# Performance work log

Measured on AMD Instinct MI355X. Metric: run time of the kernel, lower is better.

Reference implementation:

```python
import jax, jax.numpy as jnp
import numpy as np
from jax import lax

L, B, N, D = 6, 4, 2048, 512
H, DH = 8, 64
ID = H * DH           # 512
M = 266               # int(64*log(64)) random features
INNER = 2 * D         # conformer expansion
K = 31                # depthwise kernel
PAD = (15, 15)        # calc_same_padding(31)
EPS_LN = 1e-5


def setup_inputs() -> dict:
    key = jax.random.key(0)
    ks = jax.random.split(key, 12)
    s = 0.02
    return {
        "x": jax.random.normal(ks[0], (B, N, D), jnp.float32),
        "ln1_g": jnp.ones((L, D), jnp.float32),
        "ln1_b": jnp.zeros((L, D), jnp.float32),
        "wq": jax.random.normal(ks[1], (L, ID, D), jnp.float32) * s,
        "bq": jnp.zeros((L, ID), jnp.float32),
        "wk": jax.random.normal(ks[2], (L, ID, D), jnp.float32) * s,
        "bk": jnp.zeros((L, ID), jnp.float32),
        "wv": jax.random.normal(ks[3], (L, ID, D), jnp.float32) * s,
        "bv": jnp.zeros((L, ID), jnp.float32),
        "wo": jax.random.normal(ks[4], (L, ID, D), jnp.float32) * s,
        "bo": jnp.zeros((L, D), jnp.float32),
        # FAVOR+ random projection buffer (gaussian orthogonal ~ iid gaussian rows)
        "proj": jax.random.normal(ks[5], (L, M, DH), jnp.float32),
        "ln2_g": jnp.ones((L, D), jnp.float32),
        "ln2_b": jnp.zeros((L, D), jnp.float32),
        "pw1_w": jax.random.normal(ks[6], (L, 2 * INNER, D), jnp.float32) * s,
        "pw1_b": jnp.zeros((L, 2 * INNER), jnp.float32),
        "dw_w": jax.random.normal(ks[7], (L, INNER, K), jnp.float32) * s,
        "dw_b": jnp.zeros((L, INNER), jnp.float32),
        "pw2_w": jax.random.normal(ks[8], (L, D, INNER), jnp.float32) * s,
        "pw2_b": jnp.zeros((L, D), jnp.float32),
    }


def layer_norm(x, g, b):
    mu = jnp.mean(x, axis=-1, keepdims=True)
    var = jnp.mean((x - mu) ** 2, axis=-1, keepdims=True)
    return (x - mu) * lax.rsqrt(var + EPS_LN) * g + b


def softmax_kernel(data, proj, is_query, eps=1e-4):
    # data: [b,h,n,dh], proj: [m,dh]
    dn = DH ** -0.25
    ratio = M ** -0.5
    data_dash = jnp.einsum('bhnd,md->bhnm', dn * data, proj)
    diag = jnp.sum(data * data, axis=-1, keepdims=True) * 0.5 * dn * dn  # [b,h,n,1]
    if is_query:
        mx = jnp.max(data_dash, axis=-1, keepdims=True)
        return ratio * (jnp.exp(data_dash - diag - mx) + eps)
    else:
        return ratio * jnp.exp(data_dash - diag + eps)


def favor_attention(q, k, v, proj):
    qp = softmax_kernel(q, proj, True)   # [b,h,n,m]
    kp = softmax_kernel(k, proj, False)  # [b,h,n,m]
    k_cumsum = jnp.sum(kp, axis=-2)      # [b,h,m]
    d_inv = 1.0 / (jnp.einsum('bhnm,bhm->bhn', qp, k_cumsum) + 1e-8)
    context = jnp.einsum('bhnm,bhne->bhme', kp, v)          # [b,h,m,dh]
    out = jnp.einsum('bhme,bhnm,bhn->bhne', context, qp, d_inv)
    return out


def pcmer_forward(x, ln1_g, ln1_b, wq, bq, wk, bk, wv, bv, wo, bo, proj,
                  ln2_g, ln2_b, pw1_w, pw1_b, dw_w, dw_b, pw2_w, pw2_b):
    for l in range(L):
        # --- self attention (FAVOR+) ---
        h = layer_norm(x, ln1_g[l], ln1_b[l])
        q = (h @ wq[l].T + bq[l]).reshape(B, N, H, DH).transpose(0, 2, 1, 3)
        k = (h @ wk[l].T + bk[l]).reshape(B, N, H, DH).transpose(0, 2, 1, 3)
        v = (h @ wv[l].T + bv[l]).reshape(B, N, H, DH).transpose(0, 2, 1, 3)
        o = favor_attention(q, k, v, proj[l])                 # [b,h,n,dh]
        o = o.transpose(0, 2, 1, 3).reshape(B, N, ID)
        x = x + (o @ wo[l].T + bo[l])
        # --- conformer conv module ---
        h = layer_norm(x, ln2_g[l], ln2_b[l])
        y = h @ pw1_w[l].T + pw1_b[l]                         # [b,n,2*inner]
        a, g = y[..., :INNER], y[..., INNER:]
        y = a * jax.nn.sigmoid(g)                             # GLU
        yt = jnp.pad(y.transpose(0, 2, 1), ((0, 0), (0, 0), PAD))  # [b,inner,n+30]
        dw = lax.conv_general_dilated(
            yt, dw_w[l][:, None, :], window_strides=(1,), padding='VALID',
            feature_group_count=INNER,
            dimension_numbers=('NCH', 'OIH', 'NCH')) + dw_b[l][None, :, None]
        dw = jax.nn.silu(dw).transpose(0, 2, 1)               # [b,n,inner]
        x = x + (dw @ pw2_w[l].T + pw2_b[l])
    return x


def reference(x, ln1_g, ln1_b, wq, bq, wk, bk, wv, bv, wo, bo, proj,
              ln2_g, ln2_b, pw1_w, pw1_b, dw_w, dw_b, pw2_w, pw2_b):
    return pcmer_forward(x, ln1_g, ln1_b, wq, bq, wk, bk, wv, bv, wo, bo, proj,
                         ln2_g, ln2_b, pw1_w, pw1_b, dw_w, dw_b, pw2_w, pw2_b)
```

## Files before the change

kernel.cpp:

```cpp
#include <hip/hip_runtime.h>


#define L_LAYERS 6
#define B_ 4
#define N_ 2048
#define D_ 512
#define H_ 8
#define DH_ 64
#define M_ 266
#define INNER_ 1024
#define T_ 8192
#define PS_ 320
#define QKVS_ 1536
#define NS_ 8

typedef __attribute__((ext_vector_type(8))) short short8;
typedef __attribute__((ext_vector_type(4))) float floatx4;

__device__ __forceinline__ ushort f2bf(float f) {
  union { float f; uint u; } v; v.f = f;
  uint r = v.u + 0x7fffu + ((v.u >> 16) & 1u);
  return (ushort)(r >> 16);
}
__device__ __forceinline__ float bf2f(ushort u) {
  union { uint u; float f; } v; v.u = ((uint)u) << 16;
  return v.f;
}
__device__ __forceinline__ float wave_sum(float v) {
#pragma unroll
  for (int m = 1; m < 64; m <<= 1) v += __shfl_xor(v, m);
  return v;
}
__device__ __forceinline__ void async_cp16(const void* g, void* l) {
  __builtin_amdgcn_global_load_lds(
      (const __attribute__((address_space(1))) void*)g,
      (__attribute__((address_space(3))) void*)l, 16, 0, 0);
}

__global__ void f2bf4_kernel(const float4* __restrict__ in, ushort* __restrict__ out, int n4) {
  int i = blockIdx.x * 256 + threadIdx.x;
  if (i < n4) {
    float4 v = in[i];
    ushort4 r;
    r.x = f2bf(v.x); r.y = f2bf(v.y); r.z = f2bf(v.z); r.w = f2bf(v.w);
    *(ushort4*)(out + (size_t)i * 4) = r;
  }
}
__global__ void pack_qkv_w(const float4* __restrict__ src, ushort* __restrict__ dst, int off) {
  int i = blockIdx.x * 256 + threadIdx.x;
  if (i >= L_LAYERS * 512 * 128) return;
  int l = i >> 16;
  int rem = i & 65535;
  int row = rem >> 7, c4 = rem & 127;
  float4 v = src[i];
  ushort4 r;
  r.x = f2bf(v.x); r.y = f2bf(v.y); r.z = f2bf(v.z); r.w = f2bf(v.w);
  *(ushort4*)(dst + ((size_t)l * QKVS_ + off + row) * 512 + c4 * 4) = r;
}
__global__ void pack_qkv_b(const float* __restrict__ bq, const float* __restrict__ bk,
                           const float* __restrict__ bv, float* __restrict__ dst) {
  int i = blockIdx.x * 256 + threadIdx.x;
  if (i >= L_LAYERS * QKVS_) return;
  int l = i / QKVS_, c = i % QKVS_;
  dst[i] = c < 512 ? bq[l * 512 + c] : (c < 1024 ? bk[l * 512 + c - 512] : bv[l * 512 + c - 1024]);
}
__global__ void pad_proj(const float* __restrict__ proj, ushort* __restrict__ dst) {
  int i = blockIdx.x * 256 + threadIdx.x;
  if (i >= L_LAYERS * 320 * 64) return;
  int l = i / (320 * 64), rem = i % (320 * 64), m = rem >> 6, kk = rem & 63;
  dst[i] = (m < M_) ? f2bf(proj[((size_t)l * M_ + m) * 64 + kk]) : (ushort)0;
}
__global__ void pack_pw1_w(const float4* __restrict__ src, ushort* __restrict__ dst) {
  int i = blockIdx.x * 256 + threadIdx.x;
  if (i >= L_LAYERS * 2048 * 128) return;
  int l = i >> 18;
  int rem = i & 262143;
  int cp = rem >> 7, c4 = rem & 127;
  int s = (cp >> 4) & 1;
  int srow = ((cp >> 5) << 4) + (cp & 15) + s * 1024;
  float4 v = src[((size_t)l * 2048 + srow) * 128 + c4];
  ushort4 r;
  r.x = f2bf(v.x); r.y = f2bf(v.y); r.z = f2bf(v.z); r.w = f2bf(v.w);
  *(ushort4*)(dst + ((size_t)l * 2048 + cp) * 512 + c4 * 4) = r;
}
__global__ void pack_pw1_b(const float* __restrict__ src, float* __restrict__ dst) {
  int i = blockIdx.x * 256 + threadIdx.x;
  if (i >= L_LAYERS * 2048) return;
  int l = i >> 11, cp = i & 2047;
  int s = (cp >> 4) & 1;
  int srow = ((cp >> 5) << 4) + (cp & 15) + s * 1024;
  dst[i] = src[l * 2048 + srow];
}

__global__ __launch_bounds__(256) void ln_kernel(const float* __restrict__ x,
                                                 const float* __restrict__ g,
                                                 const float* __restrict__ b,
                                                 ushort* __restrict__ out) {
  const int t = blockIdx.x;
  const int tid = threadIdx.x;
  const float* row = x + (size_t)t * D_;
  float v0 = row[tid], v1 = row[tid + 256];
  float s1 = v0 + v1;
  float s2 = v0 * v0 + v1 * v1;
  s1 = wave_sum(s1);
  s2 = wave_sum(s2);
  __shared__ float sh1[4], sh2[4];
  int w = tid >> 6;
  if ((tid & 63) == 0) { sh1[w] = s1; sh2[w] = s2; }
  __syncthreads();
  s1 = sh1[0] + sh1[1] + sh1[2] + sh1[3];
  s2 = sh2[0] + sh2[1] + sh2[2] + sh2[3];
  float mu = s1 * (1.f / D_);
  float var = s2 * (1.f / D_) - mu * mu;
  float rs = rsqrtf(var + 1e-5f);
  out[(size_t)t * D_ + tid]       = f2bf((v0 - mu) * rs * g[tid] + b[tid]);
  out[(size_t)t * D_ + tid + 256] = f2bf((v1 - mu) * rs * g[tid + 256] + b[tid + 256]);
}

template <bool HAS_RES, bool OUT_BF16, int ACT, int KT>
__global__ __launch_bounds__(256) void gemm_mfma(const ushort* __restrict__ A,
                                                 const ushort* __restrict__ W,
                                                 const float* __restrict__ bias,
                                                 const float* __restrict__ res,
                                                 void* __restrict__ Cout,
                                                 int ldc) {
  constexpr int NT = KT / 32;
  __shared__ ushort As[3][128 * 32];
  __shared__ ushort Bs[3][128 * 32];
  const int tid = threadIdx.x;
  const int w = tid >> 6, lane = tid & 63;
  const int row0 = blockIdx.x * 128, col0 = blockIdx.y * 128;
  const int rl = lane >> 2;
  const int lc = ((lane & 3) ^ ((lane >> 3) & 3)) * 8;
  const ushort* gA0 = A + (size_t)(row0 + w * 32 + rl) * KT + lc;
  const ushort* gA1 = gA0 + (size_t)16 * KT;
  const ushort* gB0 = W + (size_t)(col0 + w * 32 + rl) * KT + lc;
  const ushort* gB1 = gB0 + (size_t)16 * KT;
  const int m16 = lane & 15, quad = lane >> 4;
  const int awr = (w >> 1) * 64, bwc = (w & 1) * 64;
  floatx4 acc[4][4] = {};

  auto stage = [&](int t, int buf) {
    async_cp16(gA0 + t * 32, As[buf] + w * 1024);
    async_cp16(gA1 + t * 32, As[buf] + w * 1024 + 512);
    async_cp16(gB0 + t * 32, Bs[buf] + w * 1024);
    async_cp16(gB1 + t * 32, Bs[buf] + w * 1024 + 512);
  };
  auto body = [&](int buf, bool bar2) {
    short8 af[4], bfr[4];
#pragma unroll
    for (int i = 0; i < 4; i++) {
      int r = awr + i * 16 + m16;
      af[i] = *(const short8*)&As[buf][r * 32 + (quad ^ ((r >> 1) & 3)) * 8];
    }
#pragma unroll
    for (int j = 0; j < 4; j++) {
      int r = bwc + j * 16 + m16;
      bfr[j] = *(const short8*)&Bs[buf][r * 32 + (quad ^ ((r >> 1) & 3)) * 8];
    }
    if (bar2) {
      asm volatile("s_waitcnt lgkmcnt(0)" ::: "memory");
      __builtin_amdgcn_sched_barrier(0);
      __builtin_amdgcn_s_barrier();
    }
#pragma unroll
    for (int i = 0; i < 4; i++)
#pragma unroll
      for (int j = 0; j < 4; j++)
        acc[i][j] = __builtin_amdgcn_mfma_f32_16x16x32_bf16(af[i], bfr[j], acc[i][j], 0, 0, 0);
  };

  stage(0, 0);
  stage(1, 1);
  int c = 0;
  for (int t = 0; t < NT - 2; t++) {
    int pf = c + 2; if (pf >= 3) pf -= 3;
    stage(t + 2, pf);
    asm volatile("s_waitcnt vmcnt(8)" ::: "memory");
    __builtin_amdgcn_s_barrier();
    body(c, true);
    c++; if (c >= 3) c -= 3;
  }
  asm volatile("s_waitcnt vmcnt(4)" ::: "memory");
  __builtin_amdgcn_s_barrier();
  body(c, false);
  c++; if (c >= 3) c -= 3;
  asm volatile("s_waitcnt vmcnt(0)" ::: "memory");
  __builtin_amdgcn_s_barrier();
  body(c, false);

  if (ACT == 0) {
#pragma unroll
    for (int i = 0; i < 4; i++) {
      const int r0 = row0 + awr + i * 16 + quad * 4;
#pragma unroll
      for (int j = 0; j < 4; j++) {
        const int cc = col0 + bwc + j * 16 + m16;
        const float bv = bias[cc];
#pragma unroll
        for (int r = 0; r < 4; r++) {
          float vv = acc[i][j][r] + bv;
          if (HAS_RES) vv += res[(size_t)(r0 + r) * ldc + cc];
          if (OUT_BF16) ((ushort*)Cout)[(size_t)(r0 + r) * ldc + cc] = f2bf(vv);
          else          ((float*)Cout)[(size_t)(r0 + r) * ldc + cc] = vv;
        }
      }
    }
  } else {
#pragma unroll
    for (int i = 0; i < 4; i++) {
      const int r0 = row0 + awr + i * 16 + quad * 4;
#pragma unroll
      for (int jp = 0; jp < 2; jp++) {
        const int j = jp * 2;
        const int ca = col0 + bwc + j * 16 + m16;
        const float ba = bias[ca], bg = bias[ca + 16];
        const int oc = ((col0 + bwc) >> 1) + jp * 16 + m16;
#pragma unroll
        for (int r = 0; r < 4; r++) {
          float a = acc[i][j][r] + ba;
          float g = acc[i][j + 1][r] + bg;
          float z = a / (1.f + expf(-g));
          ((ushort*)Cout)[(size_t)(r0 + r) * ldc + oc] = f2bf(z);
        }
      }
    }
  }
}

__global__ __launch_bounds__(256) void ctx_phi_mfma(const ushort* __restrict__ qkv,
                                                    const ushort* __restrict__ projp,
                                                    float* __restrict__ part,
                                                    float* __restrict__ kpart) {
  __shared__ ushort projs[64 * 64];
  __shared__ ushort kts[32 * 64];
  __shared__ ushort kps[64][40];
  __shared__ ushort vsT[64][40];
  __shared__ float diag_sh[32];
  __shared__ float kshare[4][64];
  const int bh = blockIdx.x, mt = blockIdx.y, ns = blockIdx.z;
  const int b = bh >> 3, h = bh & 7;
  const int m0 = mt * 64;
  const int tid = threadIdx.x;
  const int w = tid >> 6, lane = tid & 63, l16 = lane & 15, quad = lane >> 4;
  const int rl8 = lane >> 3;
  const int lc8 = ((lane & 7) ^ (rl8 & 7)) * 8;
#pragma unroll
  for (int j = 0; j < 2; j++) {
    const int rb = w * 16 + j * 8;
    async_cp16(projp + (size_t)(m0 + rb + rl8) * 64 + lc8, projs + rb * 64);
  }
  const int nn = tid >> 3;
  const int a8 = tid & 7;
  const int gn = nn >> 3, jn = nn & 7;
  const int pc = ((gn ^ (a8 & 3)) << 3) | jn;
  const int km = tid & 63, kg = tid >> 6;
  const float dn = 0.35355339059327373f;
  const float ratio = 0.06131393394849658f;
  floatx4 acc[4] = {};
  float ksp = 0.f;
  for (int nstep = 0; nstep < 2048 / NS_ / 32; nstep++) {
    const int n0 = ns * (2048 / NS_) + nstep * 32;
    {
      const int rb = w * 8;
      async_cp16(qkv + (size_t)(b * N_ + n0 + rb + rl8) * QKVS_ + 512 + h * 64 + lc8,
                 kts + rb * 64);
    }
    uint4 vv = *(const uint4*)(qkv + ((size_t)(b * N_ + n0 + nn)) * QKVS_ + 1024 + h * 64 + a8 * 8);
    __syncthreads();
    {
      const int r = tid >> 3;
      const int c = tid & 7;
      short8 kv8 = *(const short8*)&kts[r * 64 + c * 8];
      const ushort* u = (const ushort*)&kv8;
      float s = 0.f;
#pragma unroll
      for (int j = 0; j < 8; j++) { float f = bf2f(u[j]); s += f * f; }
      s += __shfl_xor(s, 1);
      s += __shfl_xor(s, 2);
      s += __shfl_xor(s, 4);
      if ((tid & 7) == 0) diag_sh[r] = 0.0625f * s;
    }
    {
      const ushort* ve = (const ushort*)&vv;
#pragma unroll
      for (int j = 0; j < 8; j++) vsT[a8 * 8 + j][pc] = ve[j];
    }
    __syncthreads();
    floatx4 pacc[2] = {};
#pragma unroll
    for (int s = 0; s < 2; s++) {
      const int ar = w * 16 + l16;
      short8 af = *(const short8*)&projs[ar * 64 + ((s * 4 + quad) ^ (ar & 7)) * 8];
#pragma unroll
      for (int nj = 0; nj < 2; nj++) {
        const int br = nj * 16 + l16;
        short8 bf = *(const short8*)&kts[br * 64 + ((s * 4 + quad) ^ (br & 7)) * 8];
        pacc[nj] = __builtin_amdgcn_mfma_f32_16x16x32_bf16(af, bf, pacc[nj], 0, 0, 0);
      }
    }
#pragma unroll
    for (int nj = 0; nj < 2; nj++) {
      const int n = nj * 16 + l16;
      const float dgn = diag_sh[n];
#pragma unroll
      for (int r = 0; r < 4; r++) {
        const int m = w * 16 + quad * 4 + r;
        float val = (m0 + m < M_) ? ratio * expf(dn * pacc[nj][r] - dgn + 1e-4f) : 0.f;
        kps[m][(((n >> 3) ^ ((m >> 3) & 3)) << 3) | (n & 7)] = f2bf(val);
      }
    }
    __syncthreads();
    const int am = w * 16 + l16;
    const int apg = quad ^ ((am >> 3) & 3);
    short8 af = *(const short8*)&kps[am][apg * 8];
#pragma unroll
    for (int et = 0; et < 4; et++) {
      const int be = et * 16 + l16;
      const int bpg = quad ^ ((be >> 3) & 3);
      short8 bf = *(const short8*)&vsT[be][bpg * 8];
      acc[et] = __builtin_amdgcn_mfma_f32_16x16x32_bf16(af, bf, acc[et], 0, 0, 0);
    }
    {
      short8 kr = *(const short8*)&kps[km][kg * 8];
      const ushort* ku = (const ushort*)&kr;
#pragma unroll
      for (int j = 0; j < 8; j++) ksp += bf2f(ku[j]);
    }
  }
  float* pb = part + ((size_t)(bh * NS_ + ns) * 5 + mt) * 4096;
#pragma unroll
  for (int et = 0; et < 4; et++)
#pragma unroll
    for (int r = 0; r < 4; r++)
      pb[(w * 16 + quad * 4 + r) * 64 + et * 16 + l16] = acc[et][r];
  kshare[kg][km] = ksp;
  __syncthreads();
  if (tid < 64)
    kpart[((size_t)(bh * NS_ + ns) * 5 + mt) * 64 + tid] =
        kshare[0][tid] + kshare[1][tid] + kshare[2][tid] + kshare[3][tid];
}

__global__ __launch_bounds__(256) void ctx_reduce(const float* __restrict__ part,
                                                  const float* __restrict__ kpart,
                                                  ushort* __restrict__ ctxbT,
                                                  float* __restrict__ ksum) {
  const int bh = blockIdx.x, mt = blockIdx.y;
  const int tid = threadIdx.x;
  const int w = tid >> 6, lane = tid & 63;
  for (int oc = w; oc < 8; oc += 4) {
    const int mbase = mt * 64 + oc * 8;
    if (mbase < 288) {
      float s[8] = {0.f, 0.f, 0.f, 0.f, 0.f, 0.f, 0.f, 0.f};
#pragma unroll
      for (int ns = 0; ns < NS_; ns++) {
        const float* pb = part + ((size_t)(bh * NS_ + ns) * 5 + mt) * 4096;
#pragma unroll
        for (int ml = 0; ml < 8; ml++) s[ml] += pb[(oc * 8 + ml) * 64 + lane];
      }
      ushort tmp[8];
#pragma unroll
      for (int ml = 0; ml < 8; ml++) tmp[ml] = f2bf(s[ml]);
      *(short8*)(ctxbT + ((size_t)(bh * 64 + lane)) * 288 + mbase) = *(const short8*)tmp;
    }
  }
  if (tid < 64) {
    float s = 0.f;
#pragma unroll
    for (int ns = 0; ns < NS_; ns++)
      s += kpart[((size_t)(bh * NS_ + ns) * 5 + mt) * 64 + tid];
    ksum[(size_t)bh * PS_ + mt * 64 + tid] = s;
  }
}

__global__ __launch_bounds__(256, 4) void attn_fused(const ushort* __restrict__ qkv,
                                                     const ushort* __restrict__ projp,
                                                     const ushort* __restrict__ ctxbT,
                                                     const float* __restrict__ ksum,
                                                     ushort* __restrict__ o) {
  __shared__ __align__(16) ushort sm[14336];
  __shared__ float ks_sh[288];
  __shared__ float diag_sh[64];
  ushort* As = sm;
  ushort* Bs = sm + 4096;
  ushort (*qst)[40] = (ushort(*)[40])sm;
  const int bh = blockIdx.x, b = bh >> 3, h = bh & 7;
  const int n0 = blockIdx.y * 64;
  const int tid = threadIdx.x;
  const int w = tid >> 6, lane = tid & 63, l16 = lane & 15, quad = lane >> 4;
  const int rl8 = lane >> 3;
  const int lc8 = ((lane & 7) ^ (rl8 & 7)) * 8;
#pragma unroll
  for (int j = 0; j < 2; j++) {
    const int rb = w * 16 + j * 8;
    async_cp16(qkv + (size_t)(b * N_ + n0 + rb + rl8) * QKVS_ + h * 64 + lc8, As + rb * 64);
  }
#pragma unroll
  for (int j = 0; j < 5; j++) {
    const int rb = w * 40 + j * 8;
    async_cp16(projp + (size_t)(rb + rl8) * 64 + lc8, Bs + rb * 64);
  }
  for (int i = tid; i < 288; i += 256) ks_sh[i] = ksum[(size_t)bh * PS_ + i];
  __syncthreads();
  {
    const int r = w * 16 + (lane >> 2);
    const int c0 = 2 * (lane & 3);
    float s = 0.f;
#pragma unroll
    for (int cc = 0; cc < 2; cc++) {
      short8 vv = *(const short8*)&As[r * 64 + ((c0 + cc) ^ (r & 7)) * 8];
      const ushort* u = (const ushort*)&vv;
#pragma unroll
      for (int j = 0; j < 8; j++) { float f = bf2f(u[j]); s += f * f; }
    }
    s += __shfl_xor(s, 1);
    s += __shfl_xor(s, 2);
    if ((lane & 3) == 0) diag_sh[r] = 0.0625f * s;
  }
  __syncthreads();
  float dgr[4];
#pragma unroll
  for (int r = 0; r < 4; r++) dgr[r] = diag_sh[w * 16 + quad * 4 + r];
  floatx4 acc[18];
#pragma unroll
  for (int cf = 0; cf < 18; cf++) acc[cf] = (floatx4){0.f, 0.f, 0.f, 0.f};
  const int ar = w * 16 + l16;
#pragma unroll
  for (int s = 0; s < 2; s++) {
    short8 af = *(const short8*)&As[ar * 64 + ((s * 4 + quad) ^ (ar & 7)) * 8];
#pragma unroll
    for (int cf = 0; cf < 10; cf++) {
      const int br = cf * 16 + l16;
      short8 bf = *(const short8*)&Bs[br * 64 + ((s * 4 + quad) ^ (br & 7)) * 8];
      acc[cf] = __builtin_amdgcn_mfma_f32_16x16x32_bf16(af, bf, acc[cf], 0, 0, 0);
    }
  }
  __syncthreads();
#pragma unroll
  for (int j = 0; j < 4; j++) {
    const int rb = w * 32 + j * 8;
    async_cp16(projp + (size_t)(160 + rb + rl8) * 64 + lc8, Bs + rb * 64);
  }
  __syncthreads();
#pragma unroll
  for (int s = 0; s < 2; s++) {
    short8 af = *(const short8*)&As[ar * 64 + ((s * 4 + quad) ^ (ar & 7)) * 8];
#pragma unroll
    for (int cf = 10; cf < 18; cf++) {
      const int br = (cf - 10) * 16 + l16;
      short8 bf = *(const short8*)&Bs[br * 64 + ((s * 4 + quad) ^ (br & 7)) * 8];
      acc[cf] = __builtin_amdgcn_mfma_f32_16x16x32_bf16(af, bf, acc[cf], 0, 0, 0);
    }
  }
  const float dn = 0.35355339059327373f;
  const float ratio = 0.06131393394849658f;
  float mxr[4];
#pragma unroll
  for (int r = 0; r < 4; r++) {
    float mx = -1e30f;
#pragma unroll
    for (int cf = 0; cf < 18; cf++) {
      const int col = cf * 16 + l16;
      if (col < M_) mx = fmaxf(mx, dn * acc[cf][r]);
    }
    mx = fmaxf(mx, __shfl_xor(mx, 1));
    mx = fmaxf(mx, __shfl_xor(mx, 2));
    mx = fmaxf(mx, __shfl_xor(mx, 4));
    mx = fmaxf(mx, __shfl_xor(mx, 8));
    mxr[r] = mx;
  }
  __syncthreads();
  float dacc[4] = {0.f, 0.f, 0.f, 0.f};
  floatx4 acc2[4] = {};
  const ushort* ctxrow = ctxbT + (size_t)bh * (64 * 288);
  for (int m0 = 0; m0 < 288; m0 += 32) {
    const int cf0 = m0 >> 4;
#pragma unroll
    for (int cc = 0; cc < 2; cc++) {
      const int col = m0 + cc * 16 + l16;
      const float kv = ks_sh[col];
#pragma unroll
      for (int r = 0; r < 4; r++) {
        float val = (col < M_) ? ratio * (expf(dn * acc[cf0 + cc][r] - dgr[r] - mxr[r]) + 1e-4f)
                               : 0.f;
        qst[w * 16 + quad * 4 + r][cc * 16 + l16] = f2bf(val);
        dacc[r] += val * kv;
      }
    }
    short8 af = *(const short8*)&qst[w * 16 + l16][quad * 8];
#pragma unroll
    for (int et = 0; et < 4; et++) {
      short8 bf = *(const short8*)(ctxrow + (size_t)(et * 16 + l16) * 288 + m0 + quad * 8);
      acc2[et] = __builtin_amdgcn_mfma_f32_16x16x32_bf16(af, bf, acc2[et], 0, 0, 0);
    }
  }
  float di[4];
#pragma unroll
  for (int r = 0; r < 4; r++) {
    float d = dacc[r];
    d += __shfl_xor(d, 1);
    d += __shfl_xor(d, 2);
    d += __shfl_xor(d, 4);
    d += __shfl_xor(d, 8);
    di[r] = 1.f / (d + 1e-8f);
  }
#pragma unroll
  for (int r = 0; r < 4; r++) {
    const int n = n0 + w * 16 + quad * 4 + r;
#pragma unroll
    for (int et = 0; et < 4; et++)
      o[((size_t)(b * N_ + n)) * 512 + h * 64 + et * 16 + l16] = f2bf(acc2[et][r] * di[r]);
  }
}

#define TN_ 16
__global__ __launch_bounds__(256) void dwconv_kernel(const ushort* __restrict__ x,
                                                     const float* __restrict__ w,
                                                     const float* __restrict__ bias,
                                                     ushort* __restrict__ out) {
  const int bid = blockIdx.x;
  const int cb = bid & 3;
  const int nb = (bid >> 2) & 127;
  const int b  = bid >> 9;
  const int c = cb * 256 + threadIdx.x;
  const int n0 = nb * TN_;
  float win[TN_ + 30];
#pragma unroll
  for (int i = 0; i < TN_ + 30; i++) {
    int nn = n0 + i - 15;
    win[i] = (nn >= 0 && nn < N_) ? bf2f(x[(size_t)(b * N_ + nn) * INNER_ + c]) : 0.f;
  }
  float wc[31];
#pragma unroll
  for (int kk = 0; kk < 31; kk++) wc[kk] = w[c * 31 + kk];
  const float bsv = bias[c];
#pragma unroll
  for (int j = 0; j < TN_; j++) {
    float acc = bsv;
#pragma unroll
    for (int kk = 0; kk < 31; kk++) acc += win[j + kk] * wc[kk];
    acc = acc / (1.f + expf(-acc));
    out[(size_t)(b * N_ + n0 + j) * INNER_ + c] = f2bf(acc);
  }
}

extern "C" void kernel_launch(void* const* d_in, const int* in_sizes, int n_in,
                              void* d_out, int out_size, void* d_ws, size_t ws_size,
                              hipStream_t stream) {
  const float* in_x  = (const float*)d_in[0];
  const float* ln1_g = (const float*)d_in[1];
  const float* ln1_b = (const float*)d_in[2];
  const float* wq    = (const float*)d_in[3];
  const float* bq    = (const float*)d_in[4];
  const float* wk    = (const float*)d_in[5];
  const float* bk    = (const float*)d_in[6];
  const float* wv    = (const float*)d_in[7];
  const float* bv    = (const float*)d_in[8];
  const float* wo    = (const float*)d_in[9];
  const float* bo    = (const float*)d_in[10];
  const float* proj  = (const float*)d_in[11];
  const float* ln2_g = (const float*)d_in[12];
  const float* ln2_b = (const float*)d_in[13];
  const float* pw1_w = (const float*)d_in[14];
  const float* pw1_b = (const float*)d_in[15];
  const float* dw_w  = (const float*)d_in[16];
  const float* dw_b  = (const float*)d_in[17];
  const float* pw2_w = (const float*)d_in[18];
  const float* pw2_b = (const float*)d_in[19];

  char* cur = (char*)d_ws;
  auto alloc = [&](size_t bytes) { char* p = cur; cur += (bytes + 255) & ~(size_t)255; return p; };
  float*  x    = (float*)alloc((size_t)T_ * D_ * 4);
  ushort* p    = (ushort*)alloc((size_t)T_ * INNER_ * 2 * 2);
  float*  part = (float*)alloc((size_t)32 * NS_ * 5 * 4096 * 4);
  float*  kpart= (float*)alloc((size_t)32 * NS_ * 5 * 64 * 4);
  ushort* ctxb = (ushort*)alloc((size_t)32 * 288 * 64 * 2);
  float*  ksum = (float*)alloc((size_t)32 * PS_ * 4);
  ushort* h    = (ushort*)alloc((size_t)T_ * D_ * 2);
  ushort* qkv  = (ushort*)alloc((size_t)T_ * QKVS_ * 2);
  ushort* obuf = (ushort*)alloc((size_t)T_ * D_ * 2);
  ushort* wqkv_b = (ushort*)alloc((size_t)L_LAYERS * QKVS_ * 512 * 2);
  float*  bqkv   = (float*)alloc((size_t)L_LAYERS * QKVS_ * 4);
  ushort* wo_b = (ushort*)alloc((size_t)L_LAYERS * D_ * D_ * 2);
  ushort* pjp  = (ushort*)alloc((size_t)L_LAYERS * 320 * 64 * 2);
  ushort* p1_b = (ushort*)alloc((size_t)L_LAYERS * 2048 * D_ * 2);
  float*  pb1  = (float*)alloc((size_t)L_LAYERS * 2048 * 4);
  ushort* p2_b = (ushort*)alloc((size_t)L_LAYERS * D_ * INNER_ * 2);
  ushort* glu  = p;
  ushort* conv = p + (size_t)T_ * INNER_;

  pack_qkv_w<<<(L_LAYERS * 512 * 128 + 255) / 256, 256, 0, stream>>>((const float4*)wq, wqkv_b, 0);
  pack_qkv_w<<<(L_LAYERS * 512 * 128 + 255) / 256, 256, 0, stream>>>((const float4*)wk, wqkv_b, 512);
  pack_qkv_w<<<(L_LAYERS * 512 * 128 + 255) / 256, 256, 0, stream>>>((const float4*)wv, wqkv_b, 1024);
  pack_qkv_b<<<(L_LAYERS * QKVS_ + 255) / 256, 256, 0, stream>>>(bq, bk, bv, bqkv);
  pad_proj<<<(L_LAYERS * 320 * 64 + 255) / 256, 256, 0, stream>>>(proj, pjp);
  pack_pw1_w<<<(L_LAYERS * 2048 * 128 + 255) / 256, 256, 0, stream>>>((const float4*)pw1_w, p1_b);
  pack_pw1_b<<<(L_LAYERS * 2048 + 255) / 256, 256, 0, stream>>>(pw1_b, pb1);
  {
    int n4 = L_LAYERS * D_ * D_ / 4;
    f2bf4_kernel<<<(n4 + 255) / 256, 256, 0, stream>>>((const float4*)wo, wo_b, n4);
    n4 = L_LAYERS * D_ * INNER_ / 4;
    f2bf4_kernel<<<(n4 + 255) / 256, 256, 0, stream>>>((const float4*)pw2_w, p2_b, n4);
  }

  for (int l = 0; l < L_LAYERS; l++) {
    const ushort* wqkvl = wqkv_b + (size_t)l * QKVS_ * 512;
    const ushort* wol = wo_b + (size_t)l * D_ * D_;
    const ushort* pjl = pjp + (size_t)l * 320 * 64;
    const ushort* p1l = p1_b + (size_t)l * 2048 * D_;
    const ushort* p2l = p2_b + (size_t)l * D_ * INNER_;
    const float*  dwl = dw_w + (size_t)l * INNER_ * 31;
    const float*  dwbl = dw_b + (size_t)l * INNER_;
    const float*  xin = (l == 0) ? in_x : x;
    float* xout = (l == L_LAYERS - 1) ? (float*)d_out : x;

    ln_kernel<<<T_, 256, 0, stream>>>(xin, ln1_g + l * D_, ln1_b + l * D_, h);
    gemm_mfma<false, true, 0, 512><<<dim3(T_ / 128, QKVS_ / 128), 256, 0, stream>>>(
        h, wqkvl, bqkv + (size_t)l * QKVS_, nullptr, qkv, QKVS_);
    ctx_phi_mfma<<<dim3(32, 5, NS_), 256, 0, stream>>>(qkv, pjl, part, kpart);
    ctx_reduce<<<dim3(32, 5), 256, 0, stream>>>(part, kpart, ctxb, ksum);
    attn_fused<<<dim3(32, 32), 256, 0, stream>>>(qkv, pjl, ctxb, ksum, obuf);
    gemm_mfma<true, false, 0, 512><<<dim3(T_ / 128, 4), 256, 0, stream>>>(
        obuf, wol, bo + l * D_, xin, x, D_);
    ln_kernel<<<T_, 256, 0, stream>>>(x, ln2_g + l * D_, ln2_b + l * D_, h);
    gemm_mfma<false, true, 1, 512><<<dim3(T_ / 128, 16), 256, 0, stream>>>(
        h, p1l, pb1 + (size_t)l * 2048, nullptr, glu, INNER_);
    dwconv_kernel<<<B_ * (N_ / TN_) * 4, 256, 0, stream>>>(glu, dwl, dwbl, conv);
    gemm_mfma<true, false, 0, 1024><<<dim3(T_ / 128, 4), 256, 0, stream>>>(
        conv, p2l, pw2_b + l * D_, x, xout, D_);
  }
}
```

Measured before the change: 1.227 ms.

## Add 256x128 triple-buffered GEMM for QKV and pointwise-1, widen dwconv tile

Adds a new MFMA GEMM kernel with 256x128 output tiles, a three-stage async-copy shared-memory pipeline and a single barrier per K-step. It replaces the 128x128 GEMM for the QKV projection and the GLU pointwise-1 projection. The larger tile raises operand reuse and cuts global loads per output, but it uses more shared memory and registers, and the grid becomes smaller for the 1536-wide QKV. The depthwise conv tile also grows from 16 to 32 rows, which lowers halo reloads but doubles the per-thread register window.

```diff
diff --git a/kernel.cpp b/kernel.cpp
--- a/kernel.cpp
+++ b/kernel.cpp
@@ -228,6 +228,116 @@
   }
 }
 
+template <bool OUT_BF16, int ACT, int KT>
+__global__ __launch_bounds__(256, 2) void gemm_big(const ushort* __restrict__ A,
+                                                   const ushort* __restrict__ W,
+                                                   const float* __restrict__ bias,
+                                                   void* __restrict__ Cout,
+                                                   int ldc) {
+  constexpr int NT = KT / 32;
+  __shared__ ushort As[3][256 * 32];
+  __shared__ ushort Bs[3][128 * 32];
+  const int tid = threadIdx.x;
+  const int w = tid >> 6, lane = tid & 63;
+  const int row0 = blockIdx.x * 256, col0 = blockIdx.y * 128;
+  const int rl = lane >> 2;
+  const int lc = ((lane & 3) ^ ((lane >> 3) & 3)) * 8;
+  const ushort* gA = A + (size_t)(row0 + w * 64 + rl) * KT + lc;
+  const ushort* gB = W + (size_t)(col0 + w * 32 + rl) * KT + lc;
+  const int m16 = lane & 15, quad = lane >> 4;
+  const int awr = (w >> 1) * 128;
+  const int bwc = (w & 1) * 64;
+  floatx4 acc[8][4] = {};
+
+  auto stage = [&](int t, int buf) {
+#pragma unroll
+    for (int j = 0; j < 4; j++)
+      async_cp16(gA + ((size_t)j * 16) * KT + t * 32, As[buf] + w * 2048 + j * 512);
+#pragma unroll
+    for (int j = 0; j < 2; j++)
+      async_cp16(gB + ((size_t)j * 16) * KT + t * 32, Bs[buf] + w * 1024 + j * 512);
+  };
+  auto body = [&](int buf, bool bar2) {
+    short8 af[8], bfr[4];
+#pragma unroll
+    for (int i = 0; i < 8; i++) {
+      int r = awr + i * 16 + m16;
+      af[i] = *(const short8*)&As[buf][r * 32 + (quad ^ ((r >> 1) & 3)) * 8];
+    }
+#pragma unroll
+    for (int j = 0; j < 4; j++) {
+      int r = bwc + j * 16 + m16;
+      bfr[j] = *(const short8*)&Bs[buf][r * 32 + (quad ^ ((r >> 1) & 3)) * 8];
+    }
+    if (bar2) {
+      asm volatile("s_waitcnt lgkmcnt(0)" ::: "memory");
+      __builtin_amdgcn_sched_barrier(0);
+      __builtin_amdgcn_s_barrier();
+    }
+#pragma unroll
+    for (int i = 0; i < 8; i++)
+#pragma unroll
+      for (int j = 0; j < 4; j++)
+        acc[i][j] = __builtin_amdgcn_mfma_f32_16x16x32_bf16(af[i], bfr[j], acc[i][j], 0, 0, 0);
+  };
+
+  stage(0, 0);
+  stage(1, 1);
+  int c = 0;
+  for (int t = 0; t < NT - 2; t++) {
+    int pf = c + 2; if (pf >= 3) pf -= 3;
+    stage(t + 2, pf);
+    asm volatile("s_waitcnt vmcnt(12)" ::: "memory");
+    __builtin_amdgcn_s_barrier();
+    body(c, true);
+    c++; if (c >= 3) c -= 3;
+  }
+  asm volatile("s_waitcnt vmcnt(6)" ::: "memory");
+  __builtin_amdgcn_s_barrier();
+  body(c, false);
+  c++; if (c >= 3) c -= 3;
+  asm volatile("s_waitcnt vmcnt(0)" ::: "memory");
+  __builtin_amdgcn_s_barrier();
+  body(c, false);
+
+  if (ACT == 0) {
+#pragma unroll
+    for (int i = 0; i < 8; i++) {
+      const int r0 = row0 + awr + i * 16 + quad * 4;
+#pragma unroll
+      for (int j = 0; j < 4; j++) {
+        const int cc = col0 + bwc + j * 16 + m16;
+        const float bv = bias[cc];
+#pragma unroll
+        for (int r = 0; r < 4; r++) {
+          float vv = acc[i][j][r] + bv;
+          if (OUT_BF16) ((ushort*)Cout)[(size_t)(r0 + r) * ldc + cc] = f2bf(vv);
+          else          ((float*)Cout)[(size_t)(r0 + r) * ldc + cc] = vv;
+        }
+      }
+    }
+  } else {
+#pragma unroll
+    for (int i = 0; i < 8; i++) {
+      const int r0 = row0 + awr + i * 16 + quad * 4;
+#pragma unroll
+      for (int jp = 0; jp < 2; jp++) {
+        const int j = jp * 2;
+        const int ca = col0 + bwc + j * 16 + m16;
+        const float ba = bias[ca], bg = bias[ca + 16];
+        const int oc = ((col0 + bwc) >> 1) + jp * 16 + m16;
+#pragma unroll
+        for (int r = 0; r < 4; r++) {
+          float a = acc[i][j][r] + ba;
+          float g = acc[i][j + 1][r] + bg;
+          float z = a / (1.f + expf(-g));
+          ((ushort*)Cout)[(size_t)(r0 + r) * ldc + oc] = f2bf(z);
+        }
+      }
+    }
+  }
+}
+
 __global__ __launch_bounds__(256) void ctx_phi_mfma(const ushort* __restrict__ qkv,
                                                     const ushort* __restrict__ projp,
                                                     float* __restrict__ part,
@@ -513,15 +623,15 @@
   }
 }
 
-#define TN_ 16
+#define TN_ 32
 __global__ __launch_bounds__(256) void dwconv_kernel(const ushort* __restrict__ x,
                                                      const float* __restrict__ w,
                                                      const float* __restrict__ bias,
                                                      ushort* __restrict__ out) {
   const int bid = blockIdx.x;
   const int cb = bid & 3;
-  const int nb = (bid >> 2) & 127;
-  const int b  = bid >> 9;
+  const int nb = (bid >> 2) & (N_ / TN_ - 1);
+  const int b  = bid >> 8;
   const int c = cb * 256 + threadIdx.x;
   const int n0 = nb * TN_;
   float win[TN_ + 30];
@@ -615,16 +725,16 @@
     float* xout = (l == L_LAYERS - 1) ? (float*)d_out : x;
 
     ln_kernel<<<T_, 256, 0, stream>>>(xin, ln1_g + l * D_, ln1_b + l * D_, h);
-    gemm_mfma<false, true, 0, 512><<<dim3(T_ / 128, QKVS_ / 128), 256, 0, stream>>>(
-        h, wqkvl, bqkv + (size_t)l * QKVS_, nullptr, qkv, QKVS_);
+    gemm_big<true, 0, 512><<<dim3(T_ / 256, QKVS_ / 128), 256, 0, stream>>>(
+        h, wqkvl, bqkv + (size_t)l * QKVS_, qkv, QKVS_);
     ctx_phi_mfma<<<dim3(32, 5, NS_), 256, 0, stream>>>(qkv, pjl, part, kpart);
     ctx_reduce<<<dim3(32, 5), 256, 0, stream>>>(part, kpart, ctxb, ksum);
     attn_fused<<<dim3(32, 32), 256, 0, stream>>>(qkv, pjl, ctxb, ksum, obuf);
     gemm_mfma<true, false, 0, 512><<<dim3(T_ / 128, 4), 256, 0, stream>>>(
         obuf, wol, bo + l * D_, xin, x, D_);
     ln_kernel<<<T_, 256, 0, stream>>>(x, ln2_g + l * D_, ln2_b + l * D_, h);
-    gemm_mfma<false, true, 1, 512><<<dim3(T_ / 128, 16), 256, 0, stream>>>(
-        h, p1l, pb1 + (size_t)l * 2048, nullptr, glu, INNER_);
+    gemm_big<true, 1, 512><<<dim3(T_ / 256, 16), 256, 0, stream>>>(
+        h, p1l, pb1 + (size_t)l * 2048, glu, INNER_);
     dwconv_kernel<<<B_ * (N_ / TN_) * 4, 256, 0, stream>>>(glu, dwl, dwbl, conv);
     gemm_mfma<true, false, 0, 1024><<<dim3(T_ / 128, 4), 256, 0, stream>>>(
         conv, p2l, pw2_b + l * D_, x, xout, D_);
```

Result: no change. 1.225 ms (-0.2%).
